# Kernel optimization log

Hardware: AMD Instinct MI355X
Metric: run time of the kernel (lower is better)

Reference implementation:

```python
import jax, jax.numpy as jnp
import numpy as np
import math

B, T, D = 4, 4096, 512
K_CACHE = 16

def _layernorm(x, g, b, eps=1e-5):
    mu = x.mean(-1, keepdims=True)
    var = ((x - mu) ** 2).mean(-1, keepdims=True)
    return (x - mu) / jnp.sqrt(var + eps) * g + b

def _shift1(x):
    # prepend zero along time axis, drop last: x_prev[t] = x[t-1]
    return jnp.pad(x, ((0, 0), (1, 0), (0, 0)))[:, :-1]

def mipt_parallel_scan(p, theta, inp_re, inp_im):
    # Faithful replication of the torch loop: ceil(log2(T+1)) iterations,
    # each combining with the element shifted by ONE position (as written).
    Bt, Tt, Dt = p.shape
    a_re = (1.0 - p) * jnp.cos(theta)
    a_im = (1.0 - p) * jnp.sin(theta)
    b_re, b_im = inp_re, inp_im
    mask = (jnp.arange(Tt) >= 1)[None, :, None]
    steps = math.ceil(math.log2(Tt + 1))
    for _ in range(steps):
        ar_p, ai_p = _shift1(a_re), _shift1(a_im)
        br_p, bi_p = _shift1(b_re), _shift1(b_im)
        new_a_re = a_re * ar_p - a_im * ai_p
        new_a_im = a_re * ai_p + a_im * ar_p
        new_b_re = a_re * br_p - a_im * bi_p + b_re
        new_b_im = a_re * bi_p + a_im * br_p + b_im
        a_re = jnp.where(mask, new_a_re, a_re)
        a_im = jnp.where(mask, new_a_im, a_im)
        b_re = jnp.where(mask, new_b_re, b_re)
        b_im = jnp.where(mask, new_b_im, b_im)
    return b_re, b_im

def setup_inputs() -> dict:
    key = jax.random.key(0)
    ks = jax.random.split(key, 32)
    s = 0.02
    def W(k, i, o):
        return jax.random.normal(k, (i, o), jnp.float32) * s
    inp = {
        'x': jax.random.normal(ks[0], (B, T, D), jnp.float32),
        'ln1_g': jnp.ones((D,), jnp.float32), 'ln1_b': jnp.zeros((D,), jnp.float32),
        'ln2_g': jnp.ones((D,), jnp.float32), 'ln2_b': jnp.zeros((D,), jnp.float32),
        'Wp_w': W(ks[1], D, D), 'Wp_b': jnp.zeros((D,), jnp.float32),
        'Wt_w': W(ks[2], D, D), 'Wt_b': jnp.zeros((D,), jnp.float32),
        'Wr_w': W(ks[3], D, D), 'Wr_b': jnp.zeros((D,), jnp.float32),
        'Wi_w': W(ks[4], D, D), 'Wi_b': jnp.zeros((D,), jnp.float32),
        'Wk_w': W(ks[5], D, D), 'Wk_b': jnp.zeros((D,), jnp.float32),
        'Wv_w': W(ks[6], D, D), 'Wv_b': jnp.zeros((D,), jnp.float32),
        'Wq_w': W(ks[7], D, D), 'Wq_b': jnp.zeros((D,), jnp.float32),
        'gate_w': W(ks[8], D, 1), 'gate_b': jnp.zeros((1,), jnp.float32),
        'ffn1_w': W(ks[9], D, 4 * D), 'ffn1_b': jnp.zeros((4 * D,), jnp.float32),
        'ffn2_w': W(ks[10], 4 * D, D), 'ffn2_b': jnp.zeros((D,), jnp.float32),
    }
    return inp

def reference(x, ln1_g, ln1_b, ln2_g, ln2_b, Wp_w, Wp_b, Wt_w, Wt_b, Wr_w, Wr_b,
              Wi_w, Wi_b, Wk_w, Wk_b, Wv_w, Wv_b, Wq_w, Wq_b, gate_w, gate_b,
              ffn1_w, ffn1_b, ffn2_w, ffn2_b):
    Bx, Tx, Dx = x.shape
    residual = x
    xn = _layernorm(x, ln1_g, ln1_b)
    p = jax.nn.sigmoid(xn @ Wp_w + Wp_b)
    theta = xn @ Wt_w + Wt_b
    inp_re = xn @ Wr_w + Wr_b
    inp_im = xn @ Wi_w + Wi_b
    h_re, _h_im = mipt_parallel_scan(p, theta, inp_re, inp_im)
    h_mean = h_re.mean(axis=1)  # [B, D]
    # CausalSparseCache (eval mode)
    p_scalar = p.mean(axis=-1)  # [B, T]
    K = min(K_CACHE, Tx)
    _, topk_idx = jax.lax.top_k(p_scalar, K)  # [B, K]
    idx = jnp.broadcast_to(topk_idx[:, :, None], (Bx, K, Dx))
    h_topk = jnp.take_along_axis(h_re, idx, axis=1)  # [B, K, D]
    keys = h_topk @ Wk_w + Wk_b
    values = h_topk @ Wv_w + Wv_b
    query = (h_mean @ Wq_w + Wq_b)[:, None, :]  # [B, 1, D]
    scores = jnp.einsum('bqd,bkd->bqk', query, keys) / math.sqrt(Dx)
    attn = jax.nn.softmax(scores, axis=-1)
    cache_out = jnp.einsum('bqk,bkd->bqd', attn, values)[:, 0]  # [B, D]
    g = jax.nn.sigmoid(h_mean @ gate_w + gate_b)  # [B, 1]
    out = h_mean + g * cache_out
    h = h_re + residual
    hn = _layernorm(h, ln2_g, ln2_b)
    ffn = jax.nn.gelu(hn @ ffn1_w + ffn1_b, approximate=False) @ ffn2_w + ffn2_b
    h = h + ffn
    return (h, out)
```

## Files before the change

### kernel.cpp

```cpp
#include <hip/hip_runtime.h>
#include <hip/hip_bf16.h>
#include <cstdint>
#include <cstddef>

typedef __bf16 bf16;
typedef __attribute__((ext_vector_type(8))) __bf16 bf16x8;
typedef __attribute__((ext_vector_type(4))) __bf16 bf16x4;
typedef __attribute__((ext_vector_type(4))) float f32x4;

#define BB 4
#define TT 4096
#define DD 512
#define MM (BB * TT)
#define OUT1_OFF ((size_t)MM * DD)

typedef __attribute__((address_space(1))) void as1_void;
typedef __attribute__((address_space(3))) void as3_void;

__device__ __forceinline__ void gl_lds16(const void* g, void* l) {
    __builtin_amdgcn_global_load_lds((as1_void*)(uintptr_t)g,
                                     (as3_void*)(uintptr_t)l, 16, 0, 0);
}

#define SIGM(x) (__builtin_amdgcn_rcpf(1.f + __expf(-(x))))

__global__ void transpose_bf16(const float* __restrict__ in, bf16* __restrict__ out,
                               int R, int C) {
    __shared__ float tile[32][33];
    const int c0 = blockIdx.x * 32, r0 = blockIdx.y * 32;
    const int tx = threadIdx.x, ty = threadIdx.y;
#pragma unroll
    for (int i = 0; i < 32; i += 8)
        tile[ty + i][tx] = in[(size_t)(r0 + ty + i) * C + (c0 + tx)];
    __syncthreads();
#pragma unroll
    for (int i = 0; i < 32; i += 8)
        out[(size_t)(c0 + ty + i) * R + (r0 + tx)] = (bf16)tile[tx][ty + i];
}

__global__ void pack_bias(const float* __restrict__ a, const float* __restrict__ b,
                          const float* __restrict__ c, const float* __restrict__ d,
                          float* __restrict__ o) {
    const int i = blockIdx.x * 256 + threadIdx.x;
    if (i < 2048) {
        const float* s = (i < 512) ? a : (i < 1024) ? b : (i < 1536) ? c : d;
        o[i] = s[i & 511];
    }
}

__global__ void zero_kernel(float* __restrict__ p, int n) {
    const int i = blockIdx.x * 256 + threadIdx.x;
    if (i < n) p[i] = 0.f;
}

__global__ __launch_bounds__(256) void ln_kernel(
    const float* __restrict__ X, const float* __restrict__ Xadd,
    const float* __restrict__ gw, const float* __restrict__ bw,
    bf16* __restrict__ out) {
    const int row = blockIdx.x * 4 + (threadIdx.x >> 6);
    const int lane = threadIdx.x & 63;
    const float* xr = X + (size_t)row * DD + lane * 8;
    float v[8];
    float4 v0 = *(const float4*)xr;
    float4 v1 = *(const float4*)(xr + 4);
    v[0] = v0.x; v[1] = v0.y; v[2] = v0.z; v[3] = v0.w;
    v[4] = v1.x; v[5] = v1.y; v[6] = v1.z; v[7] = v1.w;
    if (Xadd) {
        const float* ad = Xadd + (size_t)row * DD + lane * 8;
        float4 a0 = *(const float4*)ad;
        float4 a1 = *(const float4*)(ad + 4);
        v[0] += a0.x; v[1] += a0.y; v[2] += a0.z; v[3] += a0.w;
        v[4] += a1.x; v[5] += a1.y; v[6] += a1.z; v[7] += a1.w;
    }
    float s = 0.f, ss = 0.f;
#pragma unroll
    for (int i = 0; i < 8; ++i) { s += v[i]; ss += v[i] * v[i]; }
#pragma unroll
    for (int o = 32; o; o >>= 1) { s += __shfl_down(s, o); ss += __shfl_down(ss, o); }
    s = __shfl(s, 0); ss = __shfl(ss, 0);
    const float mu = s * (1.f / DD);
    const float var = ss * (1.f / DD) - mu * mu;
    const float rstd = rsqrtf(var + 1e-5f);
    bf16x8 o8;
#pragma unroll
    for (int i = 0; i < 8; ++i)
        o8[i] = (bf16)((v[i] - mu) * rstd * gw[lane * 8 + i] + bw[lane * 8 + i]);
    *(bf16x8*)(out + (size_t)row * DD + lane * 8) = o8;
}

#define MF(a_, b_, c_) c_ = __builtin_amdgcn_mfma_f32_16x16x32_bf16(a_, b_, c_, 0, 0, 0)

template <int MODE>
__global__ __launch_bounds__(256) void gemm_bt(
    const bf16* __restrict__ A, const bf16* __restrict__ Bt,
    const float* __restrict__ bias, void* __restrict__ Cout,
    void* __restrict__ Cout2,
    const float* __restrict__ add1, const float* __restrict__ add2,
    int M, int N, int K) {
    __shared__ bf16 As[2][4096];
    __shared__ bf16 Bs[2][4096];
    const int tid = threadIdx.x;
    const int lane = tid & 63;
    const int wv = tid >> 6;
    const int wr = wv >> 1, wc = wv & 1;
    const int nb = N >> 7;
    const int nwg = gridDim.x;
    int bx = blockIdx.x;
    if ((nwg & 7) == 0) bx = (bx & 7) * (nwg >> 3) + (bx >> 3);
    const int bm = bx / nb, bn = bx % nb;
    const int m0 = bm << 7, n0 = bn << 7;

    const int srow = tid >> 2;
    const int scol = (((tid & 3) ^ ((tid >> 3) & 3)) << 3);
    const bf16* Asrc = A + (size_t)(m0 + srow) * K + scol;
    const bf16* Bsrc = Bt + (size_t)(n0 + srow) * K + scol;
    const size_t rstep = (size_t)64 * K;

    const int lr = lane & 15, lg = lane >> 4;
    const int sel = ((lg ^ ((lr >> 1) & 3)) << 3);
    const int aoff = (wr * 64 + lr) * 32 + sel;
    const int boff = (wc * 64 + lr) * 32 + sel;

#define STG(buf, k0)                                                \
    do {                                                            \
        gl_lds16(Asrc + (k0),         &As[buf][wv * 512]);          \
        gl_lds16(Asrc + (k0) + rstep, &As[buf][wv * 512 + 2048]);   \
        gl_lds16(Bsrc + (k0),         &Bs[buf][wv * 512]);          \
        gl_lds16(Bsrc + (k0) + rstep, &Bs[buf][wv * 512 + 2048]);   \
    } while (0)

    f32x4 acc00 = {}, acc01 = {}, acc02 = {}, acc03 = {};
    f32x4 acc10 = {}, acc11 = {}, acc12 = {}, acc13 = {};
    f32x4 acc20 = {}, acc21 = {}, acc22 = {}, acc23 = {};
    f32x4 acc30 = {}, acc31 = {}, acc32 = {}, acc33 = {};

    const int NT = K >> 5;
    STG(0, 0);
    STG(1, 32);
    for (int t = 0; t < NT; ++t) {
        if (t + 1 < NT) asm volatile("s_waitcnt vmcnt(4)" ::: "memory");
        else            asm volatile("s_waitcnt vmcnt(0)" ::: "memory");
        __builtin_amdgcn_s_barrier();
        asm volatile("" ::: "memory");
        const bf16* Ab = As[t & 1];
        const bf16* Bb = Bs[t & 1];
        bf16x8 af0 = *(const bf16x8*)&Ab[aoff];
        bf16x8 af1 = *(const bf16x8*)&Ab[aoff + 512];
        bf16x8 af2 = *(const bf16x8*)&Ab[aoff + 1024];
        bf16x8 af3 = *(const bf16x8*)&Ab[aoff + 1536];
        bf16x8 bf0 = *(const bf16x8*)&Bb[boff];
        bf16x8 bf1 = *(const bf16x8*)&Bb[boff + 512];
        bf16x8 bf2 = *(const bf16x8*)&Bb[boff + 1024];
        bf16x8 bf3 = *(const bf16x8*)&Bb[boff + 1536];
        MF(af0, bf0, acc00); MF(af0, bf1, acc01); MF(af0, bf2, acc02); MF(af0, bf3, acc03);
        MF(af1, bf0, acc10); MF(af1, bf1, acc11); MF(af1, bf2, acc12); MF(af1, bf3, acc13);
        MF(af2, bf0, acc20); MF(af2, bf1, acc21); MF(af2, bf2, acc22); MF(af2, bf3, acc23);
        MF(af3, bf0, acc30); MF(af3, bf1, acc31); MF(af3, bf2, acc32); MF(af3, bf3, acc33);
        __builtin_amdgcn_s_barrier();
        asm volatile("" ::: "memory");
        if (t + 2 < NT) STG(t & 1, (t + 2) << 5);
    }
#undef STG

    if constexpr (MODE == 0) {
        const int cls = n0 >> 9;
        if (cls == 0) {
            const int pidx = (n0 + wc * 64) >> 6;
#define EPI0(mi, A0, A1, A2, A3)                                              \
    do {                                                                      \
        const int gmb = m0 + wr * 64 + mi * 16 + 4 * lg;                      \
        const int dbase = n0 + wc * 64 + lr;                                  \
        const float b0_ = bias[dbase], b1_ = bias[dbase + 16],                \
                    b2_ = bias[dbase + 32], b3_ = bias[dbase + 48];           \
        _Pragma("unroll")                                                     \
        for (int i = 0; i < 4; ++i) {                                         \
            const int row = gmb + i;                                          \
            const float p0 = SIGM(A0[i] + b0_);                               \
            const float p1 = SIGM(A1[i] + b1_);                               \
            const float p2 = SIGM(A2[i] + b2_);                               \
            const float p3 = SIGM(A3[i] + b3_);                               \
            bf16* ob = (bf16*)Cout + (size_t)row * 2048;                      \
            ob[(size_t)dbase * 4]        = (bf16)(1.f - p0);                  \
            ob[(size_t)(dbase + 16) * 4] = (bf16)(1.f - p1);                  \
            ob[(size_t)(dbase + 32) * 4] = (bf16)(1.f - p2);                  \
            ob[(size_t)(dbase + 48) * 4] = (bf16)(1.f - p3);                  \
            float s_ = p0 + p1 + p2 + p3;                                     \
            s_ += __shfl_xor(s_, 1); s_ += __shfl_xor(s_, 2);                 \
            s_ += __shfl_xor(s_, 4); s_ += __shfl_xor(s_, 8);                 \
            if (lr == 0) ((float*)Cout2)[(size_t)pidx * MM + row] = s_;       \
        }                                                                     \
    } while (0)
            EPI0(0, acc00, acc01, acc02, acc03);
            EPI0(1, acc10, acc11, acc12, acc13);
            EPI0(2, acc20, acc21, acc22, acc23);
            EPI0(3, acc30, acc31, acc32, acc33);
#undef EPI0
        } else {
#define EPIS(mi, ni, ACC)                                                     \
    do {                                                                      \
        const int gmb = m0 + wr * 64 + mi * 16 + 4 * lg;                      \
        const int gn = n0 + wc * 64 + ni * 16 + lr;                           \
        const int dn = gn & 511;                                              \
        const float bia = bias[gn];                                           \
        _Pragma("unroll")                                                     \
        for (int i = 0; i < 4; ++i)                                           \
            ((bf16*)Cout)[((size_t)(gmb + i) * 512 + dn) * 4 + cls] =         \
                (bf16)(ACC[i] + bia);                                         \
    } while (0)
            EPIS(0, 0, acc00); EPIS(0, 1, acc01); EPIS(0, 2, acc02); EPIS(0, 3, acc03);
            EPIS(1, 0, acc10); EPIS(1, 1, acc11); EPIS(1, 2, acc12); EPIS(1, 3, acc13);
            EPIS(2, 0, acc20); EPIS(2, 1, acc21); EPIS(2, 2, acc22); EPIS(2, 3, acc23);
            EPIS(3, 0, acc30); EPIS(3, 1, acc31); EPIS(3, 2, acc32); EPIS(3, 3, acc33);
#undef EPIS
        }
    } else {
#define EPI(mi, ni, ACC)                                                        \
    do {                                                                        \
        const int gmb = m0 + wr * 64 + mi * 16 + 4 * lg;                        \
        const int gn = n0 + wc * 64 + ni * 16 + lr;                             \
        const float bia = bias[gn];                                             \
        _Pragma("unroll")                                                       \
        for (int i = 0; i < 4; ++i) {                                           \
            float v = ACC[i] + bia;                                             \
            const int row = gmb + i;                                            \
            if (MODE == 1) {                                                    \
                const float ge = 0.5f * v * (1.0f + erff(v * 0.70710678118654752f)); \
                ((bf16*)Cout)[(size_t)row * N + gn] = (bf16)ge;                 \
            } else {                                                            \
                const size_t off = (size_t)row * N + gn;                        \
                ((float*)Cout)[off] = v + add1[off] + add2[off];                \
            }                                                                   \
        }                                                                       \
    } while (0)
        EPI(0, 0, acc00); EPI(0, 1, acc01); EPI(0, 2, acc02); EPI(0, 3, acc03);
        EPI(1, 0, acc10); EPI(1, 1, acc11); EPI(1, 2, acc12); EPI(1, 3, acc13);
        EPI(2, 0, acc20); EPI(2, 1, acc21); EPI(2, 2, acc22); EPI(2, 3, acc23);
        EPI(3, 0, acc30); EPI(3, 1, acc31); EPI(3, 2, acc32); EPI(3, 3, acc33);
#undef EPI
    }
}

__global__ __launch_bounds__(256) void pscalar_fin(const float* __restrict__ part,
                                                   float* __restrict__ ps) {
    const int i = blockIdx.x * 256 + threadIdx.x;
    float s = 0.f;
#pragma unroll
    for (int j = 0; j < 8; ++j) s += part[(size_t)j * MM + i];
    ps[i] = s * (1.f / 512.f);
}

#define SCL 32
__global__ __launch_bounds__(256) void scan_kernel(const bf16* __restrict__ lint4,
                                                   float* __restrict__ h_re) {
    const int blk = blockIdx.x;
    const int dh = blk & 1;
    const int tc = (blk >> 1) & 127;
    const int b = blk >> 8;
    const int d = dh * 256 + threadIdx.x;
    const int t0 = tc * SCL;

    float par[13], pai[13], pbr[13], pbi[13];
#pragma unroll
    for (int k = 0; k < 13; ++k) { par[k] = 0.f; pai[k] = 0.f; pbr[k] = 0.f; pbi[k] = 0.f; }

    const int warm = (tc == 0) ? 0 : 13;
    const bf16* tp = lint4 + ((size_t)(b * TT + t0 - warm) * 512 + d) * 4;
    float* pout = h_re + ((size_t)(b * TT + t0)) * DD + d;

#define XFORM(car, cai, cbr, cbi)                                        \
    const bf16x4 q_ = *(const bf16x4*)tp;                                \
    tp += 2048;                                                          \
    const float om = (float)q_[0];                                       \
    const float th = (float)q_[1];                                       \
    const float cbr = (float)q_[2];                                      \
    const float cbi = (float)q_[3];                                      \
    float fr_, sn, cs;                                                   \
    { const float rv_ = th * 0.15915494309189535f;                       \
      asm("v_fract_f32 %0, %1" : "=v"(fr_) : "v"(rv_));                  \
      asm("v_sin_f32 %0, %1" : "=v"(sn) : "v"(fr_));                     \
      asm("v_cos_f32 %0, %1" : "=v"(cs) : "v"(fr_)); }                   \
    float car = om * cs, cai = om * sn;

    for (int s = 0; s < warm; ++s) {
        XFORM(car, cai, cbr, cbi)
        float br_ = cbr, bi_ = cbi;
#pragma unroll
        for (int k = 0; k < 13; ++k) {
            const float tar = par[k], tai = pai[k], tbr = pbr[k], tbi = pbi[k];
            par[k] = car; pai[k] = cai; pbr[k] = br_; pbi[k] = bi_;
            const float nbr = car * tbr - cai * tbi + br_;
            const float nbi = car * tbi + cai * tbr + bi_;
            if (k < 12) {
                const float nar = car * tar - cai * tai;
                const float nai = car * tai + cai * tar;
                car = nar; cai = nai;
            }
            br_ = nbr; bi_ = nbi;
        }
    }

#pragma unroll 4
    for (int s = 0; s < SCL; ++s) {
        const int t = t0 + s;
        XFORM(car, cai, cbr, cbi)
        float br_ = cbr, bi_ = cbi;
        if (t == 0) {
#pragma unroll
            for (int k = 0; k < 13; ++k) { par[k] = car; pai[k] = cai; pbr[k] = br_; pbi[k] = bi_; }
        } else {
#pragma unroll
            for (int k = 0; k < 13; ++k) {
                const float tar = par[k], tai = pai[k], tbr = pbr[k], tbi = pbi[k];
                par[k] = car; pai[k] = cai; pbr[k] = br_; pbi[k] = bi_;
                const float nbr = car * tbr - cai * tbi + br_;
                const float nbi = car * tbi + cai * tbr + bi_;
                if (k < 12) {
                    const float nar = car * tar - cai * tai;
                    const float nai = car * tai + cai * tar;
                    car = nar; cai = nai;
                }
                br_ = nbr; bi_ = nbi;
            }
        }
        pout[(size_t)s * DD] = br_;
    }
#undef XFORM
}

__global__ __launch_bounds__(256) void hmean_kernel(const float* __restrict__ h_re,
                                                    float* __restrict__ hsum) {
    const int blk = blockIdx.x;
    const int b = blk >> 6;
    const int dh = (blk >> 5) & 1;
    const int tc = blk & 31;
    const int d = dh * 256 + threadIdx.x;
    float s = 0.f;
    const float* p = h_re + ((size_t)(b * TT + tc * 128)) * DD + d;
    for (int t = 0; t < 128; ++t) s += p[(size_t)t * DD];
    atomicAdd(&hsum[b * DD + d], s);
}

__global__ __launch_bounds__(256) void topk_kernel(const float* __restrict__ ps,
                                                   int* __restrict__ idx_out) {
    __shared__ float vals[TT];
    __shared__ float rv[4];
    __shared__ int ri[4];
    const int b = blockIdx.x, tid = threadIdx.x;
    for (int i = tid; i < TT; i += 256) vals[i] = ps[b * TT + i];
    __syncthreads();
    for (int kk = 0; kk < 16; ++kk) {
        float bv = -1e30f; int bi = 0x7fffffff;
        for (int i = tid; i < TT; i += 256) {
            const float v = vals[i];
            if (v > bv || (v == bv && i < bi)) { bv = v; bi = i; }
        }
#pragma unroll
        for (int o = 32; o; o >>= 1) {
            const float ov = __shfl_down(bv, o);
            const int oi = __shfl_down(bi, o);
            if (ov > bv || (ov == bv && oi < bi)) { bv = ov; bi = oi; }
        }
        const int lane = tid & 63, wid = tid >> 6;
        if (!lane) { rv[wid] = bv; ri[wid] = bi; }
        __syncthreads();
        if (!tid) {
            float fbv = rv[0]; int fbi = ri[0];
            for (int w = 1; w < 4; ++w)
                if (rv[w] > fbv || (rv[w] == fbv && ri[w] < fbi)) { fbv = rv[w]; fbi = ri[w]; }
            idx_out[b * 16 + kk] = fbi;
            vals[fbi] = -1e30f;
        }
        __syncthreads();
    }
}

__global__ __launch_bounds__(256) void kv_kernel(
    const float* __restrict__ h_re, const int* __restrict__ tki,
    const float* __restrict__ Wk, const float* __restrict__ Wkb,
    const float* __restrict__ Wv, const float* __restrict__ Wvb,
    float* __restrict__ keys, float* __restrict__ vals) {
    const int blk = blockIdx.x;
    const int b = blk >> 4, j = blk & 15;
    const int tid = threadIdx.x;
    __shared__ float hrow[512];
    const int row = tki[b * 16 + j];
    for (int i = tid; i < 512; i += 256)
        hrow[i] = h_re[((size_t)(b * TT + row)) * DD + i];
    __syncthreads();
    for (int n = tid; n < 512; n += 256) {
        float sk = Wkb[n], sv = Wvb[n];
        for (int k = 0; k < 512; ++k) {
            const float h = hrow[k];
            sk += h * Wk[(size_t)k * 512 + n];
            sv += h * Wv[(size_t)k * 512 + n];
        }
        keys[((size_t)(b * 16 + j)) * 512 + n] = sk;
        vals[((size_t)(b * 16 + j)) * 512 + n] = sv;
    }
}

__global__ __launch_bounds__(256) void attn_out_kernel(
    const float* __restrict__ hsum, const float* __restrict__ Wq,
    const float* __restrict__ Wqb, const float* __restrict__ gw,
    const float* __restrict__ gb, const float* __restrict__ keys,
    const float* __restrict__ vals, float* __restrict__ out1) {
    const int b = blockIdx.x, tid = threadIdx.x;
    const int lane = tid & 63, wid = tid >> 6;
    __shared__ float hm[512];
    __shared__ float q[512];
    __shared__ float sc[16];
    __shared__ float red[4];
    for (int d0 = tid; d0 < 512; d0 += 256)
        hm[d0] = hsum[b * 512 + d0] * (1.f / 4096.f);
    __syncthreads();
    for (int n = tid; n < 512; n += 256) {
        float s = Wqb[n];
        for (int k = 0; k < 512; ++k) s += hm[k] * Wq[(size_t)k * 512 + n];
        q[n] = s;
    }
    float gp = 0.f;
    for (int k = tid; k < 512; k += 256) gp += hm[k] * gw[k];
#pragma unroll
    for (int o = 32; o; o >>= 1) gp += __shfl_down(gp, o);
    if (!lane) red[wid] = gp;
    __syncthreads();
    const float g = 1.f / (1.f + __expf(-(red[0] + red[1] + red[2] + red[3] + gb[0])));
    for (int kk = wid; kk < 16; kk += 4) {
        float sp = 0.f;
        const float* kr = keys + ((size_t)(b * 16 + kk)) * 512;
        for (int k2 = lane; k2 < 512; k2 += 64) sp += q[k2] * kr[k2];
#pragma unroll
        for (int o = 32; o; o >>= 1) sp += __shfl_down(sp, o);
        if (!lane) sc[kk] = sp * 0.04419417382415922f;
    }
    __syncthreads();
    float mx = sc[0];
#pragma unroll
    for (int kk = 1; kk < 16; ++kk) mx = fmaxf(mx, sc[kk]);
    float den = 0.f;
    float w16[16];
#pragma unroll
    for (int kk = 0; kk < 16; ++kk) { w16[kk] = __expf(sc[kk] - mx); den += w16[kk]; }
    const float rden = 1.f / den;
    for (int d0 = tid; d0 < 512; d0 += 256) {
        float co = 0.f;
#pragma unroll
        for (int kk = 0; kk < 16; ++kk)
            co += w16[kk] * vals[((size_t)(b * 16 + kk)) * 512 + d0];
        out1[b * 512 + d0] = hm[d0] + g * (co * rden);
    }
}

extern "C" void kernel_launch(void* const* d_in, const int* in_sizes, int n_in,
                              void* d_out, int out_size, void* d_ws, size_t ws_size,
                              hipStream_t stream) {
    const float* x    = (const float*)d_in[0];
    const float* ln1g = (const float*)d_in[1];
    const float* ln1b = (const float*)d_in[2];
    const float* ln2g = (const float*)d_in[3];
    const float* ln2b = (const float*)d_in[4];
    const float* Wp_w = (const float*)d_in[5];
    const float* Wp_b = (const float*)d_in[6];
    const float* Wt_w = (const float*)d_in[7];
    const float* Wt_b = (const float*)d_in[8];
    const float* Wr_w = (const float*)d_in[9];
    const float* Wr_b = (const float*)d_in[10];
    const float* Wi_w = (const float*)d_in[11];
    const float* Wi_b = (const float*)d_in[12];
    const float* Wk_w = (const float*)d_in[13];
    const float* Wk_b = (const float*)d_in[14];
    const float* Wv_w = (const float*)d_in[15];
    const float* Wv_b = (const float*)d_in[16];
    const float* Wq_w = (const float*)d_in[17];
    const float* Wq_b = (const float*)d_in[18];
    const float* gw   = (const float*)d_in[19];
    const float* gb   = (const float*)d_in[20];
    const float* f1w  = (const float*)d_in[21];
    const float* f1b  = (const float*)d_in[22];
    const float* f2w  = (const float*)d_in[23];
    const float* f2b  = (const float*)d_in[24];

    char* wsp = (char*)d_ws;
    bf16* lint4 = (bf16*)wsp;
    char* p = wsp + 67108864;
    float* h_re = (float*)p; p += 33554432;
    bf16* xn = (bf16*)p;     p += 16777216;
    bf16* hn = (bf16*)p;     p += 16777216;
    bf16* wcat = (bf16*)p;   p += 2097152;
    bf16* f1bt = (bf16*)p;   p += 2097152;
    bf16* f2bt = (bf16*)p;   p += 2097152;
    float* bcat = (float*)p; p += 8192;
    float* ps = (float*)p;   p += 65536;
    float* pspart = (float*)p; p += 524288;
    float* hsum = (float*)p; p += 8192;
    int* tki = (int*)p;      p += 256;
    float* keys = (float*)p; p += 131072;
    float* valsb = (float*)p;
    bf16* act = (bf16*)wsp;
    float* out0 = (float*)d_out;
    float* out1 = (float*)d_out + OUT1_OFF;

    dim3 tb(32, 8);
    transpose_bf16<<<dim3(16, 16), tb, 0, stream>>>(Wp_w, wcat + (size_t)0 * 512 * 512, 512, 512);
    transpose_bf16<<<dim3(16, 16), tb, 0, stream>>>(Wt_w, wcat + (size_t)1 * 512 * 512, 512, 512);
    transpose_bf16<<<dim3(16, 16), tb, 0, stream>>>(Wr_w, wcat + (size_t)2 * 512 * 512, 512, 512);
    transpose_bf16<<<dim3(16, 16), tb, 0, stream>>>(Wi_w, wcat + (size_t)3 * 512 * 512, 512, 512);
    transpose_bf16<<<dim3(64, 16), tb, 0, stream>>>(f1w, f1bt, 512, 2048);
    transpose_bf16<<<dim3(16, 64), tb, 0, stream>>>(f2w, f2bt, 2048, 512);
    pack_bias<<<8, 256, 0, stream>>>(Wp_b, Wt_b, Wr_b, Wi_b, bcat);

    ln_kernel<<<4096, 256, 0, stream>>>(x, nullptr, ln1g, ln1b, xn);
    gemm_bt<0><<<2048, 256, 0, stream>>>(xn, wcat, bcat, lint4, pspart, nullptr, nullptr, MM, 2048, 512);
    pscalar_fin<<<64, 256, 0, stream>>>(pspart, ps);
    scan_kernel<<<1024, 256, 0, stream>>>(lint4, h_re);
    zero_kernel<<<8, 256, 0, stream>>>(hsum, 2048);
    hmean_kernel<<<256, 256, 0, stream>>>(h_re, hsum);
    topk_kernel<<<4, 256, 0, stream>>>(ps, tki);
    kv_kernel<<<64, 256, 0, stream>>>(h_re, tki, Wk_w, Wk_b, Wv_w, Wv_b, keys, valsb);
    attn_out_kernel<<<4, 256, 0, stream>>>(hsum, Wq_w, Wq_b, gw, gb, keys, valsb, out1);
    ln_kernel<<<4096, 256, 0, stream>>>(h_re, x, ln2g, ln2b, hn);
    gemm_bt<1><<<2048, 256, 0, stream>>>(hn, f1bt, f1b, act, nullptr, nullptr, nullptr, MM, 2048, 512);
    gemm_bt<2><<<512, 256, 0, stream>>>(act, f2bt, f2b, out0, nullptr, h_re, x, MM, 512, 2048);
}
```

Baseline: 419.5 us.

## Triple-buffer GEMM LDS pipeline and fuse time-mean reduction into scan

The GEMM main loop moves from double to triple LDS buffering. This removes the second barrier per k-step, so the next tile's global-to-LDS loads are issued before the MFMAs instead of after them. The h_mean sum is accumulated inside the scan kernel and added atomically, which removes a separate kernel that re-read the full h_re tensor. In exchange, LDS use per block grows by half, which may lower occupancy.

```diff
diff --git a/kernel.cpp b/kernel.cpp
--- a/kernel.cpp
+++ b/kernel.cpp
@@ -97,8 +97,8 @@
     void* __restrict__ Cout2,
     const float* __restrict__ add1, const float* __restrict__ add2,
     int M, int N, int K) {
-    __shared__ bf16 As[2][4096];
-    __shared__ bf16 Bs[2][4096];
+    __shared__ bf16 As[3][4096];
+    __shared__ bf16 Bs[3][4096];
     const int tid = threadIdx.x;
     const int lane = tid & 63;
     const int wv = tid >> 6;
@@ -137,13 +137,14 @@
     const int NT = K >> 5;
     STG(0, 0);
     STG(1, 32);
+    int cur = 0;
     for (int t = 0; t < NT; ++t) {
         if (t + 1 < NT) asm volatile("s_waitcnt vmcnt(4)" ::: "memory");
         else            asm volatile("s_waitcnt vmcnt(0)" ::: "memory");
         __builtin_amdgcn_s_barrier();
         asm volatile("" ::: "memory");
-        const bf16* Ab = As[t & 1];
-        const bf16* Bb = Bs[t & 1];
+        const bf16* Ab = As[cur];
+        const bf16* Bb = Bs[cur];
         bf16x8 af0 = *(const bf16x8*)&Ab[aoff];
         bf16x8 af1 = *(const bf16x8*)&Ab[aoff + 512];
         bf16x8 af2 = *(const bf16x8*)&Ab[aoff + 1024];
@@ -152,13 +153,15 @@
         bf16x8 bf1 = *(const bf16x8*)&Bb[boff + 512];
         bf16x8 bf2 = *(const bf16x8*)&Bb[boff + 1024];
         bf16x8 bf3 = *(const bf16x8*)&Bb[boff + 1536];
+        if (t + 2 < NT) {
+            const int stg = (cur == 0) ? 2 : cur - 1;
+            STG(stg, (t + 2) << 5);
+        }
         MF(af0, bf0, acc00); MF(af0, bf1, acc01); MF(af0, bf2, acc02); MF(af0, bf3, acc03);
         MF(af1, bf0, acc10); MF(af1, bf1, acc11); MF(af1, bf2, acc12); MF(af1, bf3, acc13);
         MF(af2, bf0, acc20); MF(af2, bf1, acc21); MF(af2, bf2, acc22); MF(af2, bf3, acc23);
         MF(af3, bf0, acc30); MF(af3, bf1, acc31); MF(af3, bf2, acc32); MF(af3, bf3, acc33);
-        __builtin_amdgcn_s_barrier();
-        asm volatile("" ::: "memory");
-        if (t + 2 < NT) STG(t & 1, (t + 2) << 5);
+        cur = (cur == 2) ? 0 : cur + 1;
     }
 #undef STG
 
@@ -251,7 +254,8 @@
 
 #define SCL 32
 __global__ __launch_bounds__(256) void scan_kernel(const bf16* __restrict__ lint4,
-                                                   float* __restrict__ h_re) {
+                                                   float* __restrict__ h_re,
+                                                   float* __restrict__ hsum) {
     const int blk = blockIdx.x;
     const int dh = blk & 1;
     const int tc = (blk >> 1) & 127;
@@ -299,6 +303,7 @@
         }
     }
 
+    float hacc = 0.f;
 #pragma unroll 4
     for (int s = 0; s < SCL; ++s) {
         const int t = t0 + s;
@@ -323,21 +328,10 @@
             }
         }
         pout[(size_t)s * DD] = br_;
+        hacc += br_;
     }
 #undef XFORM
-}
-
-__global__ __launch_bounds__(256) void hmean_kernel(const float* __restrict__ h_re,
-                                                    float* __restrict__ hsum) {
-    const int blk = blockIdx.x;
-    const int b = blk >> 6;
-    const int dh = (blk >> 5) & 1;
-    const int tc = blk & 31;
-    const int d = dh * 256 + threadIdx.x;
-    float s = 0.f;
-    const float* p = h_re + ((size_t)(b * TT + tc * 128)) * DD + d;
-    for (int t = 0; t < 128; ++t) s += p[(size_t)t * DD];
-    atomicAdd(&hsum[b * DD + d], s);
+    atomicAdd(&hsum[b * DD + d], hacc);
 }
 
 __global__ __launch_bounds__(256) void topk_kernel(const float* __restrict__ ps,
@@ -512,9 +506,8 @@
     ln_kernel<<<4096, 256, 0, stream>>>(x, nullptr, ln1g, ln1b, xn);
     gemm_bt<0><<<2048, 256, 0, stream>>>(xn, wcat, bcat, lint4, pspart, nullptr, nullptr, MM, 2048, 512);
     pscalar_fin<<<64, 256, 0, stream>>>(pspart, ps);
-    scan_kernel<<<1024, 256, 0, stream>>>(lint4, h_re);
     zero_kernel<<<8, 256, 0, stream>>>(hsum, 2048);
-    hmean_kernel<<<256, 256, 0, stream>>>(h_re, hsum);
+    scan_kernel<<<1024, 256, 0, stream>>>(lint4, h_re, hsum);
     topk_kernel<<<4, 256, 0, stream>>>(ps, tki);
     kv_kernel<<<64, 256, 0, stream>>>(h_re, tki, Wk_w, Wk_b, Wv_w, Wv_b, keys, valsb);
     attn_out_kernel<<<4, 256, 0, stream>>>(hsum, Wq_w, Wq_b, gw, gb, keys, valsb, out1);
```

Measured after the change: 409.6 us. -2.4%, faster.
